# Performance work log

Hardware: AMD Instinct MI355X
Metric: run time of the kernel (lower is better)

Reference implementation:

```python
import jax, jax.numpy as jnp
import numpy as np

B, H, S, DK = 4, 16, 1024, 64
DROP_P = 0.5

def setup_inputs() -> dict:
    key = jax.random.key(0)
    kq, kk, kv, km, kt, kd = jax.random.split(key, 6)
    Q = jax.random.normal(kq, (B, H, S, DK), dtype=jnp.float32)
    K = jax.random.normal(kk, (B, H, S, DK), dtype=jnp.float32)
    V = jax.random.normal(kv, (B, H, S, DK), dtype=jnp.float32)
    attn_mask = jax.random.randint(km, (B, H, S, S), 0, 2).astype(jnp.bool_)
    time_weight = jax.random.uniform(kt, (B, H, S, S), dtype=jnp.float32)
    drop_u = jax.random.uniform(kd, (B, H, S, S), dtype=jnp.float32)
    return {"Q": Q, "K": K, "V": V, "attn_mask": attn_mask,
            "time_weight": time_weight, "drop_u": drop_u}

def reference(Q, K, V, attn_mask, time_weight, drop_u):
    scale = 1.0 / np.sqrt(DK).astype(np.float32)
    # [B,H,S,S] scores
    scores = jnp.einsum('bhqd,bhkd->bhqk', Q, K) * scale
    scores = jnp.where(attn_mask, jnp.float32(-1e9), scores)
    attn = jax.nn.softmax(scores, axis=-1)
    attn = attn * time_weight
    # dropout(p=0.5), training mode: keep where u >= p, scale by 1/(1-p)
    keep = (drop_u >= DROP_P).astype(attn.dtype)
    attn = attn * keep * (1.0 / (1.0 - DROP_P))
    context = jnp.einsum('bhqk,bhkd->bhqd', attn, V)
    return context
```

## Files before the change

kernel.cpp:

```cpp
#include <hip/hip_runtime.h>
#include <hip/hip_bf16.h>

#define S 1024
#define DK 64
#define NKT (S / 64)
#define PITCH 72

typedef __attribute__((ext_vector_type(8))) short short8;
typedef __attribute__((ext_vector_type(4))) float f32x4;
typedef __attribute__((ext_vector_type(4))) unsigned short u16x4;

__device__ __forceinline__ unsigned short f2bf(float x) {
    unsigned int u = __float_as_uint(x);
    u += 0x7fffu + ((u >> 16) & 1u);
    return (unsigned short)(u >> 16);
}
__device__ __forceinline__ float bf2f(unsigned short h) {
    return __uint_as_float(((unsigned int)h) << 16);
}

__global__ __launch_bounds__(256, 2)
void attn_fused(const float* __restrict__ Q, const float* __restrict__ K,
                const float* __restrict__ V, const int* __restrict__ mask,
                const float* __restrict__ tw, const float* __restrict__ du,
                float* __restrict__ out) {
    const int tid  = threadIdx.x;
    const int wave = tid >> 6;
    const int lane = tid & 63;
    const int l15  = lane & 15;
    const int quad = lane >> 4;

    const int bh = blockIdx.x >> 4;
    const int qt = blockIdx.x & 15;

    __shared__ unsigned short Kh[64 * PITCH];
    __shared__ unsigned short Kl[64 * PITCH];
    __shared__ unsigned short Vh[64 * PITCH];
    __shared__ unsigned short Vl[64 * PITCH];
    __shared__ unsigned short Pb[64 * PITCH];

    short8 qh[2], ql[2];
    {
        const float* qg =
            Q + ((size_t)bh * S + (size_t)(qt * 64 + wave * 16 + l15)) * DK + quad * 8;
#pragma unroll
        for (int c = 0; c < 2; ++c) {
            float4 a = ((const float4*)(qg + c * 32))[0];
            float4 b = ((const float4*)(qg + c * 32))[1];
            float v[8] = {a.x, a.y, a.z, a.w, b.x, b.y, b.z, b.w};
#pragma unroll
            for (int j = 0; j < 8; ++j) {
                float x = v[j] * 0.125f;
                unsigned short h = f2bf(x);
                qh[c][j] = (short)h;
                ql[c][j] = (short)f2bf(x - bf2f(h));
            }
        }
    }

    const size_t rowq = (size_t)bh * S + (size_t)(qt * 64 + wave * 16 + quad * 4);
    const int*   mp  = mask + rowq * S + l15;
    const float* twp = tw   + rowq * S + l15;
    const float* dup = du   + rowq * S + l15;

    float m_run[4], l_run[4];
    f32x4 Oacc[4];
#pragma unroll
    for (int r = 0; r < 4; ++r) { m_run[r] = -3.0e38f; l_run[r] = 0.f; }
#pragma unroll
    for (int t = 0; t < 4; ++t) Oacc[t] = (f32x4){0.f, 0.f, 0.f, 0.f};

#pragma unroll 1
    for (int kt = 0; kt < NKT; ++kt) {
        __syncthreads();
        {
            const int row = tid >> 2;
            const int cp  = (tid & 3) << 4;
            const float* kg = K + ((size_t)bh * S + (size_t)(kt * 64 + row)) * DK + cp;
            const float* vg = V + ((size_t)bh * S + (size_t)(kt * 64 + row)) * DK + cp;
#pragma unroll
            for (int i = 0; i < 4; ++i) {
                float4 kv = ((const float4*)kg)[i];
                float ke[4] = {kv.x, kv.y, kv.z, kv.w};
                u16x4 h4, l4;
#pragma unroll
                for (int j = 0; j < 4; ++j) {
                    unsigned short h = f2bf(ke[j]);
                    h4[j] = h;
                    l4[j] = f2bf(ke[j] - bf2f(h));
                }
                *(u16x4*)&Kh[row * PITCH + cp + i * 4] = h4;
                *(u16x4*)&Kl[row * PITCH + cp + i * 4] = l4;

                float4 vv = ((const float4*)vg)[i];
                float ve[4] = {vv.x, vv.y, vv.z, vv.w};
#pragma unroll
                for (int j = 0; j < 4; ++j) {
                    int d = cp + i * 4 + j;
                    unsigned short h = f2bf(ve[j]);
                    Vh[d * PITCH + row] = h;
                    Vl[d * PITCH + row] = f2bf(ve[j] - bf2f(h));
                }
            }
        }
        __syncthreads();

        f32x4 sc[4];
#pragma unroll
        for (int t = 0; t < 4; ++t) {
            f32x4 acc = (f32x4){0.f, 0.f, 0.f, 0.f};
#pragma unroll
            for (int c = 0; c < 2; ++c) {
                const int ba = (t * 16 + l15) * PITCH + c * 32 + quad * 8;
                short8 bh8 = *(const short8*)&Kh[ba];
                short8 bl8 = *(const short8*)&Kl[ba];
                acc = __builtin_amdgcn_mfma_f32_16x16x32_bf16(qh[c], bh8, acc, 0, 0, 0);
                acc = __builtin_amdgcn_mfma_f32_16x16x32_bf16(ql[c], bh8, acc, 0, 0, 0);
                acc = __builtin_amdgcn_mfma_f32_16x16x32_bf16(qh[c], bl8, acc, 0, 0, 0);
            }
            sc[t] = acc;
        }

        float pw[4][4];
        float alpha[4];
#pragma unroll
        for (int r = 0; r < 4; ++r) {
            const size_t off0 = (size_t)r * S + (size_t)(kt * 64);
            int mk[4]; float twv[4], duv[4];
#pragma unroll
            for (int t = 0; t < 4; ++t) {
                mk[t]  = mp [off0 + t * 16];
                twv[t] = twp[off0 + t * 16];
                duv[t] = dup[off0 + t * 16];
            }
            float s[4];
#pragma unroll
            for (int t = 0; t < 4; ++t) s[t] = mk[t] ? -1e9f : sc[t][r];
            float rm = fmaxf(fmaxf(s[0], s[1]), fmaxf(s[2], s[3]));
#pragma unroll
            for (int off = 8; off >= 1; off >>= 1) rm = fmaxf(rm, __shfl_xor(rm, off));
            const float mn = fmaxf(m_run[r], rm);
            const float al = __expf(m_run[r] - mn);
            float ps = 0.f;
#pragma unroll
            for (int t = 0; t < 4; ++t) {
                float pe = __expf(s[t] - mn);
                ps += pe;
                float w = (duv[t] >= 0.5f) ? (twv[t] + twv[t]) : 0.f;
                pw[r][t] = pe * w;
            }
#pragma unroll
            for (int off = 8; off >= 1; off >>= 1) ps += __shfl_xor(ps, off);
            l_run[r] = l_run[r] * al + ps;
            m_run[r] = mn;
            alpha[r] = al;
        }
#pragma unroll
        for (int t = 0; t < 4; ++t)
#pragma unroll
            for (int r = 0; r < 4; ++r) Oacc[t][r] *= alpha[r];

        unsigned short phs[4][4];
#pragma unroll
        for (int r = 0; r < 4; ++r)
#pragma unroll
            for (int t = 0; t < 4; ++t) {
                unsigned short h = f2bf(pw[r][t]);
                phs[r][t] = h;
                Pb[(wave * 16 + quad * 4 + r) * PITCH + t * 16 + l15] = h;
            }
        const int pab = (wave * 16 + l15) * PITCH + quad * 8;
        short8 ah[2], alf[2];
        ah[0] = *(const short8*)&Pb[pab];
        ah[1] = *(const short8*)&Pb[pab + 32];
#pragma unroll
        for (int r = 0; r < 4; ++r)
#pragma unroll
            for (int t = 0; t < 4; ++t)
                Pb[(wave * 16 + quad * 4 + r) * PITCH + t * 16 + l15] =
                    f2bf(pw[r][t] - bf2f(phs[r][t]));
        alf[0] = *(const short8*)&Pb[pab];
        alf[1] = *(const short8*)&Pb[pab + 32];

#pragma unroll
        for (int t = 0; t < 4; ++t) {
            f32x4 o = Oacc[t];
#pragma unroll
            for (int c = 0; c < 2; ++c) {
                const int vb = (t * 16 + l15) * PITCH + c * 32 + quad * 8;
                short8 vh8 = *(const short8*)&Vh[vb];
                short8 vl8 = *(const short8*)&Vl[vb];
                o = __builtin_amdgcn_mfma_f32_16x16x32_bf16(ah[c],  vh8, o, 0, 0, 0);
                o = __builtin_amdgcn_mfma_f32_16x16x32_bf16(alf[c], vh8, o, 0, 0, 0);
                o = __builtin_amdgcn_mfma_f32_16x16x32_bf16(ah[c],  vl8, o, 0, 0, 0);
            }
            Oacc[t] = o;
        }
    }

    const size_t ob =
        ((size_t)bh * S + (size_t)(qt * 64 + wave * 16 + quad * 4)) * DK + l15;
#pragma unroll
    for (int r = 0; r < 4; ++r) {
        const float inv = 1.0f / l_run[r];
#pragma unroll
        for (int t = 0; t < 4; ++t)
            out[ob + (size_t)r * DK + t * 16] = Oacc[t][r] * inv;
    }
}

extern "C" void kernel_launch(void* const* d_in, const int* in_sizes, int n_in,
                              void* d_out, int out_size, void* d_ws, size_t ws_size,
                              hipStream_t stream) {
    const float* Q  = (const float*)d_in[0];
    const float* K  = (const float*)d_in[1];
    const float* V  = (const float*)d_in[2];
    const int*   M  = (const int*)  d_in[3];
    const float* TW = (const float*)d_in[4];
    const float* DU = (const float*)d_in[5];
    float* out = (float*)d_out;

    dim3 grid(4 * 16 * (S / 64));
    attn_fused<<<grid, dim3(256), 0, stream>>>(Q, K, V, M, TW, DU, out);
}
```

Before: 772.2 us.

## Prefetch next K/V tile and mask/weight/dropout loads into registers

Software-pipelines the global loads. The K/V tile and the per-row mask, time-weight and dropout values for the next key tile are issued into registers one iteration early, so their latency overlaps the current tile's softmax and PV MFMAs. The __syncthreads calls become LDS-only waitcnt plus s_barrier, so outstanding global prefetches do not stall the barrier. Launch bounds move to 3 blocks per CU, which caps register use while the prefetch buffers add register pressure, so spilling is a risk. The final iteration issues a wrapped, unused prefetch.

```diff
diff --git a/kernel.cpp b/kernel.cpp
--- a/kernel.cpp
+++ b/kernel.cpp
@@ -19,7 +19,13 @@
     return __uint_as_float(((unsigned int)h) << 16);
 }
 
-__global__ __launch_bounds__(256, 2)
+#define LGKM_BARRIER()                                         \
+    do {                                                       \
+        asm volatile("s_waitcnt lgkmcnt(0)" ::: "memory");     \
+        __builtin_amdgcn_s_barrier();                          \
+    } while (0)
+
+__global__ __launch_bounds__(256, 3)
 void attn_fused(const float* __restrict__ Q, const float* __restrict__ K,
                 const float* __restrict__ V, const int* __restrict__ mask,
                 const float* __restrict__ tw, const float* __restrict__ du,
@@ -63,6 +69,40 @@
     const float* twp = tw   + rowq * S + l15;
     const float* dup = du   + rowq * S + l15;
 
+    const int srow = tid >> 2;
+    const int scp  = (tid & 3) << 4;
+    const float* Kb = K + (size_t)bh * S * DK + (size_t)srow * DK + scp;
+    const float* Vb = V + (size_t)bh * S * DK + (size_t)srow * DK + scp;
+
+    float4 Gk[4], Gv[4];
+    int    mkv[4][4];
+    float  twv[4][4], duv[4][4];
+
+#define ISSUE_KV(KT)                                                         \
+    do {                                                                     \
+        const float* kg_ = Kb + (size_t)(KT) * 64 * DK;                      \
+        const float* vg_ = Vb + (size_t)(KT) * 64 * DK;                      \
+        _Pragma("unroll") for (int i_ = 0; i_ < 4; ++i_) {                   \
+            Gk[i_] = ((const float4*)kg_)[i_];                               \
+            Gv[i_] = ((const float4*)vg_)[i_];                               \
+        }                                                                    \
+    } while (0)
+
+#define ISSUE_SIDE(KT)                                                      \
+    do {                                                                    \
+        _Pragma("unroll") for (int r_ = 0; r_ < 4; ++r_) {                  \
+            const size_t o_ = (size_t)r_ * S + (size_t)((KT) * 64);         \
+            _Pragma("unroll") for (int t_ = 0; t_ < 4; ++t_) {              \
+                mkv[r_][t_] = mp [o_ + t_ * 16];                            \
+                twv[r_][t_] = twp[o_ + t_ * 16];                            \
+                duv[r_][t_] = dup[o_ + t_ * 16];                            \
+            }                                                               \
+        }                                                                   \
+    } while (0)
+
+    ISSUE_KV(0);
+    ISSUE_SIDE(0);
+
     float m_run[4], l_run[4];
     f32x4 Oacc[4];
 #pragma unroll
@@ -72,16 +112,11 @@
 
 #pragma unroll 1
     for (int kt = 0; kt < NKT; ++kt) {
-        __syncthreads();
+        LGKM_BARRIER();
         {
-            const int row = tid >> 2;
-            const int cp  = (tid & 3) << 4;
-            const float* kg = K + ((size_t)bh * S + (size_t)(kt * 64 + row)) * DK + cp;
-            const float* vg = V + ((size_t)bh * S + (size_t)(kt * 64 + row)) * DK + cp;
 #pragma unroll
             for (int i = 0; i < 4; ++i) {
-                float4 kv = ((const float4*)kg)[i];
-                float ke[4] = {kv.x, kv.y, kv.z, kv.w};
+                float ke[4] = {Gk[i].x, Gk[i].y, Gk[i].z, Gk[i].w};
                 u16x4 h4, l4;
 #pragma unroll
                 for (int j = 0; j < 4; ++j) {
@@ -89,21 +124,20 @@
                     h4[j] = h;
                     l4[j] = f2bf(ke[j] - bf2f(h));
                 }
-                *(u16x4*)&Kh[row * PITCH + cp + i * 4] = h4;
-                *(u16x4*)&Kl[row * PITCH + cp + i * 4] = l4;
-
-                float4 vv = ((const float4*)vg)[i];
-                float ve[4] = {vv.x, vv.y, vv.z, vv.w};
+                *(u16x4*)&Kh[srow * PITCH + scp + i * 4] = h4;
+                *(u16x4*)&Kl[srow * PITCH + scp + i * 4] = l4;
+
+                float ve[4] = {Gv[i].x, Gv[i].y, Gv[i].z, Gv[i].w};
 #pragma unroll
                 for (int j = 0; j < 4; ++j) {
-                    int d = cp + i * 4 + j;
+                    int d = scp + i * 4 + j;
                     unsigned short h = f2bf(ve[j]);
-                    Vh[d * PITCH + row] = h;
-                    Vl[d * PITCH + row] = f2bf(ve[j] - bf2f(h));
+                    Vh[d * PITCH + srow] = h;
+                    Vl[d * PITCH + srow] = f2bf(ve[j] - bf2f(h));
                 }
             }
         }
-        __syncthreads();
+        LGKM_BARRIER();
 
         f32x4 sc[4];
 #pragma unroll
@@ -121,21 +155,16 @@
             sc[t] = acc;
         }
 
+        const int ktn = (kt + 1) & (NKT - 1);
+        ISSUE_KV(ktn);
+
         float pw[4][4];
         float alpha[4];
 #pragma unroll
         for (int r = 0; r < 4; ++r) {
-            const size_t off0 = (size_t)r * S + (size_t)(kt * 64);
-            int mk[4]; float twv[4], duv[4];
-#pragma unroll
-            for (int t = 0; t < 4; ++t) {
-                mk[t]  = mp [off0 + t * 16];
-                twv[t] = twp[off0 + t * 16];
-                duv[t] = dup[off0 + t * 16];
-            }
             float s[4];
 #pragma unroll
-            for (int t = 0; t < 4; ++t) s[t] = mk[t] ? -1e9f : sc[t][r];
+            for (int t = 0; t < 4; ++t) s[t] = mkv[r][t] ? -1e9f : sc[t][r];
             float rm = fmaxf(fmaxf(s[0], s[1]), fmaxf(s[2], s[3]));
 #pragma unroll
             for (int off = 8; off >= 1; off >>= 1) rm = fmaxf(rm, __shfl_xor(rm, off));
@@ -146,7 +175,7 @@
             for (int t = 0; t < 4; ++t) {
                 float pe = __expf(s[t] - mn);
                 ps += pe;
-                float w = (duv[t] >= 0.5f) ? (twv[t] + twv[t]) : 0.f;
+                float w = (duv[r][t] >= 0.5f) ? (twv[r][t] + twv[r][t]) : 0.f;
                 pw[r][t] = pe * w;
             }
 #pragma unroll
@@ -155,6 +184,9 @@
             m_run[r] = mn;
             alpha[r] = al;
         }
+
+        ISSUE_SIDE(ktn);
+
 #pragma unroll
         for (int t = 0; t < 4; ++t)
 #pragma unroll
```

Result: no change. 762.0 us (-1.3%).
